# Optimization experiments

Hardware: AMD Instinct MI355X
Metric: run time of the kernel (lower is better)

Reference implementation:

```python
import jax, jax.numpy as jnp
import numpy as np

H = 200  # LSTM hidden size
DT = 48  # tactile dim
DA = 6   # action dim


def setup_inputs() -> dict:
    key = jax.random.key(0)
    ks = jax.random.split(key, 16)
    T, B = 20, 32768
    s = 0.05
    inp = {
        "tactiles": jax.random.normal(ks[0], (T, B, DT), jnp.float32),
        "actions": jax.random.normal(ks[1], (T, B, DA), jnp.float32),
        # lstm1: input 48 -> hidden 200 (PyTorch gate order i,f,g,o)
        "Wih1": jax.random.normal(ks[2], (4 * H, DT), jnp.float32) * s,
        "Whh1": jax.random.normal(ks[3], (4 * H, H), jnp.float32) * s,
        "bih1": jax.random.normal(ks[4], (4 * H,), jnp.float32) * s,
        "bhh1": jax.random.normal(ks[5], (4 * H,), jnp.float32) * s,
        # lstm2: input 248 -> hidden 200
        "Wih2": jax.random.normal(ks[6], (4 * H, H + DT), jnp.float32) * s,
        "Whh2": jax.random.normal(ks[7], (4 * H, H), jnp.float32) * s,
        "bih2": jax.random.normal(ks[8], (4 * H,), jnp.float32) * s,
        "bhh2": jax.random.normal(ks[9], (4 * H,), jnp.float32) * s,
        # fc1: 248 -> 200, fc2: 200 -> 48
        "W1": jax.random.normal(ks[10], (H, H + DT), jnp.float32) * s,
        "b1": jax.random.normal(ks[11], (H,), jnp.float32) * s,
        "W2": jax.random.normal(ks[12], (DT, H), jnp.float32) * s,
        "b2": jax.random.normal(ks[13], (DT,), jnp.float32) * s,
        "context_frames": 10,
    }
    return inp


def _lstm_cell(x, h, c, Wih, Whh, b):
    z = x @ Wih.T + h @ Whh.T + b
    i, f, g, o = jnp.split(z, 4, axis=-1)
    c = jax.nn.sigmoid(f) * c + jax.nn.sigmoid(i) * jnp.tanh(g)
    h = jax.nn.sigmoid(o) * jnp.tanh(c)
    return h, c


def reference(tactiles, actions, Wih1, Whh1, bih1, bhh1, Wih2, Whh2, bih2, bhh2, W1, b1, W2, b2, context_frames):
    T, B, _ = tactiles.shape
    cf = int(context_frames)
    state = actions[0]  # [B, DA]
    bb1 = bih1 + bhh1
    bb2 = bih2 + bhh2

    def tiled(a):
        return jnp.concatenate([a, state, a, state, a, state, a, state], axis=-1)

    def body(carry, inp, prev_tact):
        h1, c1, h2, c2, _ = carry
        act = inp[1] if prev_tact is None else inp
        x1 = inp[0] if prev_tact is None else prev_tact
        h1, c1 = _lstm_cell(x1, h1, c1, Wih1, Whh1, bb1)
        x2 = jnp.concatenate([h1, tiled(act)], axis=-1)  # [B, 248]
        h2, c2 = _lstm_cell(x2, h2, c2, Wih2, Whh2, bb2)
        lp = jnp.concatenate([h2, x1], axis=-1)  # [B, 248]
        out3 = jnp.tanh(lp @ W1.T + b1)
        out4 = jnp.tanh(out3 @ W2.T + b2)
        return (h1, c1, h2, c2, out4)

    def ctx_step(carry, inp):
        return body(carry, inp, None), None

    def pred_step(carry, act):
        new = body(carry, act, carry[4])
        return new, new[4]

    z = jnp.zeros((B, H), tactiles.dtype)
    carry0 = (z, z, z, z, jnp.zeros((B, DT), tactiles.dtype))
    # context phase: indices 0..cf-1 feed ground-truth tactile
    carry, _ = jax.lax.scan(ctx_step, carry0, (tactiles[:cf], actions[1:cf + 1]))
    last_output = carry[4]
    # prediction phase: indices cf..T-2 feed previous prediction
    carry, preds = jax.lax.scan(pred_step, carry, actions[cf + 1:T])
    return jnp.concatenate([last_output[None], preds], axis=0)  # [T-cf, B, 48]
```

## Files before the change

kernel.cpp:

```cpp
#include <hip/hip_runtime.h>


typedef short bf16x8 __attribute__((ext_vector_type(8)));
typedef float f32x16 __attribute__((ext_vector_type(16)));

#define NFRAG    1398
#define FRAG_B2  448
#define FRAG_BF1 1260
#define FRAG_BF2 1372

__device__ __forceinline__ unsigned short f2bf(float f) {
  unsigned int x = __float_as_uint(f);
  x += 0x7fffu + ((x >> 16) & 1u);
  return (unsigned short)(x >> 16);
}
__device__ __forceinline__ float sigf(float x) {
  return __builtin_amdgcn_rcpf(1.f + __expf(-x));
}
__device__ __forceinline__ float tanh_f(float x) {
  float e = __expf(2.f * fabsf(x));
  float t = 1.f - 2.f * __builtin_amdgcn_rcpf(e + 1.f);
  return copysignf(t, x);
}

__device__ __forceinline__ const bf16x8* uni_frag(
    const unsigned short* __restrict__ ws, int frag) {
  const int f = __builtin_amdgcn_readfirstlane(frag);
  return (const bf16x8*)(ws + (size_t)f * 512);
}

__global__ void actp_prep(
    const float* __restrict__ Wih1, const float* __restrict__ Whh1,
    const float* __restrict__ bih1, const float* __restrict__ bhh1,
    const float* __restrict__ Wih2, const float* __restrict__ Whh2,
    const float* __restrict__ bih2, const float* __restrict__ bhh2,
    const float* __restrict__ W1,   const float* __restrict__ W2,
    unsigned short* __restrict__ ws)
{
  const int bid = blockIdx.x, l = threadIdx.x;
  if (bid >= NFRAG) {
    const int idx = (bid - NFRAG) * 64 + l;
    float* bb = (float*)(ws + (size_t)NFRAG * 512);
    if (idx < 800)        bb[idx] = bih1[idx] + bhh1[idx];
    else if (idx < 1600)  bb[idx] = bih2[idx - 800] + bhh2[idx - 800];
    return;
  }
  const int ncol = l & 31;
  const int kb   = (l >> 5) * 8;
  float v[8];
  if (bid < FRAG_B2) {
    int t = bid; const int g = t / 112; t -= g * 112;
    const int jt = t / 16, kc = t % 16;
    const int n = jt * 32 + ncol, row = g * 200 + n;
#pragma unroll
    for (int i = 0; i < 8; ++i) {
      const int k = kc * 16 + kb + i; float val = 0.f;
      if (n < 200) {
        if (kc < 3) val = Wih1[row * 48 + k];
        else { const int kk = k - 48; if (kk < 200) val = Whh1[row * 200 + kk]; }
      }
      v[i] = val;
    }
  } else if (bid < FRAG_BF1) {
    int t = bid - FRAG_B2; const int g = t / 203; t -= g * 203;
    const int jt = t / 29, kc = t % 29;
    const int n = jt * 32 + ncol, row = g * 200 + n;
#pragma unroll
    for (int i = 0; i < 8; ++i) {
      const int k = kc * 16 + kb + i; float val = 0.f;
      if (n < 200) {
        if (kc < 13)      { if (k < 200) val = Wih2[row * 248 + k]; }
        else if (kc < 16) { val = Wih2[row * 248 + 200 + (k - 208)]; }
        else { const int kk = k - 256; if (kk < 200) val = Whh2[row * 200 + kk]; }
      }
      v[i] = val;
    }
  } else if (bid < FRAG_BF2) {
    int t = bid - FRAG_BF1; const int jt = t / 16, kc = t % 16;
    const int n = jt * 32 + ncol;
#pragma unroll
    for (int i = 0; i < 8; ++i) {
      const int k = kc * 16 + kb + i; float val = 0.f;
      if (n < 200) {
        if (kc < 13) { if (k < 200) val = W1[n * 248 + k]; }
        else         val = W1[n * 248 + 200 + (k - 208)];
      }
      v[i] = val;
    }
  } else {
    int t = bid - FRAG_BF2; const int jt = t / 13, kc = t % 13;
    const int n = jt * 32 + ncol;
#pragma unroll
    for (int i = 0; i < 8; ++i) {
      const int k = kc * 16 + kb + i; float val = 0.f;
      if (n < 48 && k < 200) val = W2[n * 200 + k];
      v[i] = val;
    }
  }
  bf16x8 o;
#pragma unroll
  for (int i = 0; i < 8; ++i) o[i] = (short)f2bf(v[i]);
  ((bf16x8*)ws)[(size_t)bid * 64 + l] = o;
}

template<int KC, int C1, int C2>
__device__ __forceinline__ f32x16 gemm1g(
    const unsigned short* __restrict__ A1, int S1,
    const unsigned short* __restrict__ A2, int S2,
    const unsigned short* __restrict__ A3, int S3,
    const bf16x8* __restrict__ B, int lane)
{
  const int r32 = lane & 31, ao = (lane >> 5) * 8;
#define APTR(kc) ((kc) < C1 ? (A1 + r32 * S1 + (kc) * 16 + ao) \
               : ((kc) < C2 ? (A2 + r32 * S2 + ((kc) - C1) * 16 + ao) \
                            : (A3 + r32 * S3 + ((kc) - C2) * 16 + ao)))
  f32x16 acc;
#pragma unroll
  for (int r = 0; r < 16; ++r) acc[r] = 0.f;
  bf16x8 a[4];
#pragma unroll
  for (int p = 0; p < 4 && p < KC; ++p) a[p] = *(const bf16x8*)APTR(p);
  bf16x8 b[8];
#pragma unroll
  for (int p = 0; p < 8 && p < KC; ++p) b[p] = B[(size_t)p * 64 + lane];
#pragma unroll
  for (int kc = 0; kc < KC; ++kc) {
    acc = __builtin_amdgcn_mfma_f32_32x32x16_bf16(a[kc & 3], b[kc & 7], acc, 0, 0, 0);
    if (kc + 4 < KC) a[kc & 3] = *(const bf16x8*)APTR(kc + 4);
    if (kc + 8 < KC) b[kc & 7] = B[(size_t)(kc + 8) * 64 + lane];
  }
#undef APTR
  return acc;
}

__global__ __launch_bounds__(512)
__attribute__((amdgpu_waves_per_eu(2)))
void actp_main(
    const float* __restrict__ tact, const float* __restrict__ act,
    const unsigned short* __restrict__ ws,
    const float* __restrict__ b1v, const float* __restrict__ b2v,
    float* __restrict__ out)
{
  __shared__ unsigned short lds[32768];
  unsigned short* const h1bufA = lds;
  unsigned short* const h1bufB = lds + 7424;
  unsigned short* const h2bufA = lds + 14848;
  unsigned short* const h2bufB = lds + 22272;
  unsigned short* const x1b    = lds + 29696;
  unsigned short* const tld    = lds + 31232;

  const int tid = threadIdx.x, lane = tid & 63, wid = tid >> 6;
  const int q = wid;
  const int l31 = lane & 31, kh = lane >> 5;
  const int jc = q * 32 + l31;
  const size_t rowbase = (size_t)blockIdx.x * 32;

  const float* const bb1 = (const float*)(ws + (size_t)NFRAG * 512);
  const float* const bb2 = bb1 + 800;
  const bool vv = jc < 200;

  for (int i = tid; i < 3712; i += 512) {
    ((unsigned int*)h1bufB)[i] = 0u;
    ((unsigned int*)h2bufB)[i] = 0u;
  }

  float c1[16], c2[16], tmp[16];
#pragma unroll
  for (int r = 0; r < 16; ++r) { c1[r] = 0.f; c2[r] = 0.f; }

  for (int s = 0; s < 19; ++s) {
    if (s < 10 && tid < 192) {
      const int row = tid / 6, ch = tid % 6;
      const float* src = tact + ((size_t)s * 32768 + rowbase + row) * 48 + ch * 8;
      float4 v0 = *(const float4*)src;
      float4 v1 = *(const float4*)(src + 4);
      bf16x8 u;
      u[0] = (short)f2bf(v0.x); u[1] = (short)f2bf(v0.y);
      u[2] = (short)f2bf(v0.z); u[3] = (short)f2bf(v0.w);
      u[4] = (short)f2bf(v1.x); u[5] = (short)f2bf(v1.y);
      u[6] = (short)f2bf(v1.z); u[7] = (short)f2bf(v1.w);
      *(bf16x8*)(x1b + row * 48 + ch * 8) = u;
    }
    if (tid < 64) {
      const int row = tid >> 1, hf = tid & 1;
      const float* pa = act + ((size_t)(s + 1) * 32768 + rowbase + row) * 6;
      const float* ps = act + (rowbase + row) * 6;
      float a6[6], s6[6];
#pragma unroll
      for (int j = 0; j < 6; ++j) { a6[j] = pa[j]; s6[j] = ps[j]; }
#pragma unroll
      for (int k = 0; k < 3; ++k) {
        bf16x8 w;
#pragma unroll
        for (int j = 0; j < 8; ++j) {
          const int c = k * 8 + j;
          const int b6 = c / 6, jj = c % 6;
          w[j] = (short)f2bf((b6 & 1) ? s6[jj] : a6[jj]);
        }
        *(bf16x8*)(tld + row * 48 + hf * 24 + k * 8) = w;
      }
    }
    __syncthreads();

    const int P = s & 1;
    unsigned short* const h1n = P ? h1bufB : h1bufA;
    unsigned short* const h1o = P ? h1bufA : h1bufB;
    unsigned short* const h2n = P ? h2bufB : h2bufA;
    unsigned short* const h2o = P ? h2bufA : h2bufB;

    if (q < 7) {
      {
        const float bf = vv ? bb1[200 + jc] : 0.f;
        f32x16 z = gemm1g<16, 3, 16>(x1b, 48, h1o, 232, h1o, 232,
                                     uni_frag(ws, 112 + q * 16), lane);
#pragma unroll
        for (int r = 0; r < 16; ++r) c1[r] *= sigf(z[r] + bf);
      }
      {
        const float bi = vv ? bb1[jc] : 0.f;
        f32x16 z = gemm1g<16, 3, 16>(x1b, 48, h1o, 232, h1o, 232,
                                     uni_frag(ws, q * 16), lane);
#pragma unroll
        for (int r = 0; r < 16; ++r) tmp[r] = sigf(z[r] + bi);
      }
      {
        const float bg = vv ? bb1[400 + jc] : 0.f;
        f32x16 z = gemm1g<16, 3, 16>(x1b, 48, h1o, 232, h1o, 232,
                                     uni_frag(ws, 224 + q * 16), lane);
#pragma unroll
        for (int r = 0; r < 16; ++r) c1[r] += tmp[r] * tanh_f(z[r] + bg);
      }
      {
        const float bo = vv ? bb1[600 + jc] : 0.f;
        f32x16 z = gemm1g<16, 3, 16>(x1b, 48, h1o, 232, h1o, 232,
                                     uni_frag(ws, 336 + q * 16), lane);
#pragma unroll
        for (int r = 0; r < 16; ++r) {
          const int row = 4 * kh + 8 * (r >> 2) + (r & 3);
          h1n[row * 232 + jc] = f2bf(sigf(z[r] + bo) * tanh_f(c1[r]));
        }
      }
    }
    __syncthreads();

    if (q < 7) {
      {
        const float bf = vv ? bb2[200 + jc] : 0.f;
        f32x16 z = gemm1g<29, 13, 16>(h1n, 232, tld, 48, h2o, 232,
                                      uni_frag(ws, FRAG_B2 + 203 + q * 29), lane);
#pragma unroll
        for (int r = 0; r < 16; ++r) c2[r] *= sigf(z[r] + bf);
      }
      {
        const float bi = vv ? bb2[jc] : 0.f;
        f32x16 z = gemm1g<29, 13, 16>(h1n, 232, tld, 48, h2o, 232,
                                      uni_frag(ws, FRAG_B2 + q * 29), lane);
#pragma unroll
        for (int r = 0; r < 16; ++r) tmp[r] = sigf(z[r] + bi);
      }
      {
        const float bg = vv ? bb2[400 + jc] : 0.f;
        f32x16 z = gemm1g<29, 13, 16>(h1n, 232, tld, 48, h2o, 232,
                                      uni_frag(ws, FRAG_B2 + 406 + q * 29), lane);
#pragma unroll
        for (int r = 0; r < 16; ++r) c2[r] += tmp[r] * tanh_f(z[r] + bg);
      }
      {
        const float bo = vv ? bb2[600 + jc] : 0.f;
        f32x16 z = gemm1g<29, 13, 16>(h1n, 232, tld, 48, h2o, 232,
                                      uni_frag(ws, FRAG_B2 + 609 + q * 29), lane);
#pragma unroll
        for (int r = 0; r < 16; ++r) {
          const int row = 4 * kh + 8 * (r >> 2) + (r & 3);
          h2n[row * 232 + jc] = f2bf(sigf(z[r] + bo) * tanh_f(c2[r]));
        }
      }
    }
    __syncthreads();

    if (s >= 9) {
      unsigned short* const o3 = h1o;
      if (wid < 7) {
        const float br = vv ? b1v[jc] : 0.f;
        f32x16 a = gemm1g<16, 13, 16>(h2n, 232, x1b, 48, x1b, 48,
                                      uni_frag(ws, FRAG_BF1 + wid * 16), lane);
#pragma unroll
        for (int r = 0; r < 16; ++r) {
          const int row = 4 * kh + 8 * (r >> 2) + (r & 3);
          o3[row * 232 + jc] = f2bf(tanh_f(a[r] + br));
        }
      }
      __syncthreads();
      if (wid < 2) {
        const float br = (jc < 48) ? b2v[jc] : 0.f;
        f32x16 a = gemm1g<13, 13, 13>(o3, 232, o3, 232, o3, 232,
                                      uni_frag(ws, FRAG_BF2 + wid * 13), lane);
        if (jc < 48) {
#pragma unroll
          for (int r = 0; r < 16; ++r) {
            const int row = 4 * kh + 8 * (r >> 2) + (r & 3);
            const float v = tanh_f(a[r] + br);
            out[((size_t)(s - 9) * 32768 + rowbase + row) * 48 + jc] = v;
            x1b[row * 48 + jc] = f2bf(v);
          }
        }
      }
      __syncthreads();
    }
  }
}

extern "C" void kernel_launch(void* const* d_in, const int* in_sizes, int n_in,
                              void* d_out, int out_size, void* d_ws, size_t ws_size,
                              hipStream_t stream) {
  const float* tactp = (const float*)d_in[0];
  const float* actp  = (const float*)d_in[1];
  const float* Wih1  = (const float*)d_in[2];
  const float* Whh1  = (const float*)d_in[3];
  const float* bih1  = (const float*)d_in[4];
  const float* bhh1  = (const float*)d_in[5];
  const float* Wih2  = (const float*)d_in[6];
  const float* Whh2  = (const float*)d_in[7];
  const float* bih2  = (const float*)d_in[8];
  const float* bhh2  = (const float*)d_in[9];
  const float* W1    = (const float*)d_in[10];
  const float* b1    = (const float*)d_in[11];
  const float* W2    = (const float*)d_in[12];
  const float* b2    = (const float*)d_in[13];
  unsigned short* ws = (unsigned short*)d_ws;
  float* outp = (float*)d_out;

  actp_prep<<<NFRAG + 25, 64, 0, stream>>>(Wih1, Whh1, bih1, bhh1,
                                           Wih2, Whh2, bih2, bhh2, W1, W2, ws);
  actp_main<<<1024, 512, 0, stream>>>(tactp, actp, ws, b1, b2, outp);
}
```

Baseline: 1.537 ms.

## Process 64 batch rows per block so each weight fragment feeds two MFMAs

Each block now handles 64 batch rows instead of 32. The GEMM helper computes two 32-row accumulator tiles that share every loaded weight fragment, which halves weight-fragment traffic per row and halves the grid to 512 blocks. LDS use doubles to 128 KB of dynamic shared memory, and register pressure rises because cell states and accumulators are duplicated. The A-operand prefetch depth also drops from 4 to 2 chunks. The risks are lower occupancy, possible spills, and fewer blocks to spread across the CUs.

```diff
diff --git a/kernel.cpp b/kernel.cpp
--- a/kernel.cpp
+++ b/kernel.cpp
@@ -104,33 +104,39 @@
 }
 
 template<int KC, int C1, int C2>
-__device__ __forceinline__ f32x16 gemm1g(
+__device__ __forceinline__ void gemm2m(
     const unsigned short* __restrict__ A1, int S1,
     const unsigned short* __restrict__ A2, int S2,
     const unsigned short* __restrict__ A3, int S3,
-    const bf16x8* __restrict__ B, int lane)
+    const bf16x8* __restrict__ B, f32x16* acc, int lane)
 {
   const int r32 = lane & 31, ao = (lane >> 5) * 8;
-#define APTR(kc) ((kc) < C1 ? (A1 + r32 * S1 + (kc) * 16 + ao) \
-               : ((kc) < C2 ? (A2 + r32 * S2 + ((kc) - C1) * 16 + ao) \
-                            : (A3 + r32 * S3 + ((kc) - C2) * 16 + ao)))
-  f32x16 acc;
-#pragma unroll
-  for (int r = 0; r < 16; ++r) acc[r] = 0.f;
-  bf16x8 a[4];
-#pragma unroll
-  for (int p = 0; p < 4 && p < KC; ++p) a[p] = *(const bf16x8*)APTR(p);
+#define APTR(kc, t) ((kc) < C1 ? (A1 + ((t) * 32 + r32) * S1 + (kc) * 16 + ao) \
+               : ((kc) < C2 ? (A2 + ((t) * 32 + r32) * S2 + ((kc) - C1) * 16 + ao) \
+                            : (A3 + ((t) * 32 + r32) * S3 + ((kc) - C2) * 16 + ao)))
+#pragma unroll
+  for (int r = 0; r < 16; ++r) { acc[0][r] = 0.f; acc[1][r] = 0.f; }
+  bf16x8 a0[2], a1[2];
+  a0[0] = *(const bf16x8*)APTR(0, 0);
+  a1[0] = *(const bf16x8*)APTR(0, 1);
+  if (KC > 1) {
+    a0[1] = *(const bf16x8*)APTR(1, 0);
+    a1[1] = *(const bf16x8*)APTR(1, 1);
+  }
   bf16x8 b[8];
 #pragma unroll
   for (int p = 0; p < 8 && p < KC; ++p) b[p] = B[(size_t)p * 64 + lane];
 #pragma unroll
   for (int kc = 0; kc < KC; ++kc) {
-    acc = __builtin_amdgcn_mfma_f32_32x32x16_bf16(a[kc & 3], b[kc & 7], acc, 0, 0, 0);
-    if (kc + 4 < KC) a[kc & 3] = *(const bf16x8*)APTR(kc + 4);
+    acc[0] = __builtin_amdgcn_mfma_f32_32x32x16_bf16(a0[kc & 1], b[kc & 7], acc[0], 0, 0, 0);
+    acc[1] = __builtin_amdgcn_mfma_f32_32x32x16_bf16(a1[kc & 1], b[kc & 7], acc[1], 0, 0, 0);
+    if (kc + 2 < KC) {
+      a0[kc & 1] = *(const bf16x8*)APTR(kc + 2, 0);
+      a1[kc & 1] = *(const bf16x8*)APTR(kc + 2, 1);
+    }
     if (kc + 8 < KC) b[kc & 7] = B[(size_t)(kc + 8) * 64 + lane];
   }
 #undef APTR
-  return acc;
 }
 
 __global__ __launch_bounds__(512)
@@ -141,35 +147,37 @@
     const float* __restrict__ b1v, const float* __restrict__ b2v,
     float* __restrict__ out)
 {
-  __shared__ unsigned short lds[32768];
+  extern __shared__ unsigned short lds[];
   unsigned short* const h1bufA = lds;
-  unsigned short* const h1bufB = lds + 7424;
-  unsigned short* const h2bufA = lds + 14848;
-  unsigned short* const h2bufB = lds + 22272;
-  unsigned short* const x1b    = lds + 29696;
-  unsigned short* const tld    = lds + 31232;
+  unsigned short* const h1bufB = lds + 14848;
+  unsigned short* const h2bufA = lds + 29696;
+  unsigned short* const h2bufB = lds + 44544;
+  unsigned short* const x1b    = lds + 59392;
+  unsigned short* const tld    = lds + 62464;
 
   const int tid = threadIdx.x, lane = tid & 63, wid = tid >> 6;
   const int q = wid;
   const int l31 = lane & 31, kh = lane >> 5;
   const int jc = q * 32 + l31;
-  const size_t rowbase = (size_t)blockIdx.x * 32;
+  const size_t rowbase = (size_t)blockIdx.x * 64;
 
   const float* const bb1 = (const float*)(ws + (size_t)NFRAG * 512);
   const float* const bb2 = bb1 + 800;
   const bool vv = jc < 200;
 
-  for (int i = tid; i < 3712; i += 512) {
+  for (int i = tid; i < 7424; i += 512) {
     ((unsigned int*)h1bufB)[i] = 0u;
     ((unsigned int*)h2bufB)[i] = 0u;
   }
 
-  float c1[16], c2[16], tmp[16];
-#pragma unroll
-  for (int r = 0; r < 16; ++r) { c1[r] = 0.f; c2[r] = 0.f; }
+  float c1[2][16], c2[2][16], tmp[2][16];
+#pragma unroll
+  for (int t = 0; t < 2; ++t)
+#pragma unroll
+    for (int r = 0; r < 16; ++r) { c1[t][r] = 0.f; c2[t][r] = 0.f; }
 
   for (int s = 0; s < 19; ++s) {
-    if (s < 10 && tid < 192) {
+    if (s < 10 && tid < 384) {
       const int row = tid / 6, ch = tid % 6;
       const float* src = tact + ((size_t)s * 32768 + rowbase + row) * 48 + ch * 8;
       float4 v0 = *(const float4*)src;
@@ -181,7 +189,7 @@
       u[6] = (short)f2bf(v1.z); u[7] = (short)f2bf(v1.w);
       *(bf16x8*)(x1b + row * 48 + ch * 8) = u;
     }
-    if (tid < 64) {
+    if (tid < 128) {
       const int row = tid >> 1, hf = tid & 1;
       const float* pa = act + ((size_t)(s + 1) * 32768 + rowbase + row) * 6;
       const float* ps = act + (rowbase + row) * 6;
@@ -209,71 +217,89 @@
     unsigned short* const h2o = P ? h2bufA : h2bufB;
 
     if (q < 7) {
+      f32x16 z[2];
       {
         const float bf = vv ? bb1[200 + jc] : 0.f;
-        f32x16 z = gemm1g<16, 3, 16>(x1b, 48, h1o, 232, h1o, 232,
-                                     uni_frag(ws, 112 + q * 16), lane);
-#pragma unroll
-        for (int r = 0; r < 16; ++r) c1[r] *= sigf(z[r] + bf);
+        gemm2m<16, 3, 16>(x1b, 48, h1o, 232, h1o, 232,
+                          uni_frag(ws, 112 + q * 16), z, lane);
+#pragma unroll
+        for (int t = 0; t < 2; ++t)
+#pragma unroll
+          for (int r = 0; r < 16; ++r) c1[t][r] *= sigf(z[t][r] + bf);
       }
       {
         const float bi = vv ? bb1[jc] : 0.f;
-        f32x16 z = gemm1g<16, 3, 16>(x1b, 48, h1o, 232, h1o, 232,
-                                     uni_frag(ws, q * 16), lane);
-#pragma unroll
-        for (int r = 0; r < 16; ++r) tmp[r] = sigf(z[r] + bi);
+        gemm2m<16, 3, 16>(x1b, 48, h1o, 232, h1o, 232,
+                          uni_frag(ws, q * 16), z, lane);
+#pragma unroll
+        for (int t = 0; t < 2; ++t)
+#pragma unroll
+          for (int r = 0; r < 16; ++r) tmp[t][r] = sigf(z[t][r] + bi);
       }
       {
         const float bg = vv ? bb1[400 + jc] : 0.f;
-        f32x16 z = gemm1g<16, 3, 16>(x1b, 48, h1o, 232, h1o, 232,
-                                     uni_frag(ws, 224 + q * 16), lane);
-#pragma unroll
-        for (int r = 0; r < 16; ++r) c1[r] += tmp[r] * tanh_f(z[r] + bg);
+        gemm2m<16, 3, 16>(x1b, 48, h1o, 232, h1o, 232,
+                          uni_frag(ws, 224 + q * 16), z, lane);
+#pragma unroll
+        for (int t = 0; t < 2; ++t)
+#pragma unroll
+          for (int r = 0; r < 16; ++r) c1[t][r] += tmp[t][r] * tanh_f(z[t][r] + bg);
       }
       {
         const float bo = vv ? bb1[600 + jc] : 0.f;
-        f32x16 z = gemm1g<16, 3, 16>(x1b, 48, h1o, 232, h1o, 232,
-                                     uni_frag(ws, 336 + q * 16), lane);
-#pragma unroll
-        for (int r = 0; r < 16; ++r) {
-          const int row = 4 * kh + 8 * (r >> 2) + (r & 3);
-          h1n[row * 232 + jc] = f2bf(sigf(z[r] + bo) * tanh_f(c1[r]));
-        }
+        gemm2m<16, 3, 16>(x1b, 48, h1o, 232, h1o, 232,
+                          uni_frag(ws, 336 + q * 16), z, lane);
+#pragma unroll
+        for (int t = 0; t < 2; ++t)
+#pragma unroll
+          for (int r = 0; r < 16; ++r) {
+            const int row = t * 32 + 4 * kh + 8 * (r >> 2) + (r & 3);
+            h1n[row * 232 + jc] = f2bf(sigf(z[t][r] + bo) * tanh_f(c1[t][r]));
+          }
       }
     }
     __syncthreads();
 
     if (q < 7) {
+      f32x16 z[2];
       {
         const float bf = vv ? bb2[200 + jc] : 0.f;
-        f32x16 z = gemm1g<29, 13, 16>(h1n, 232, tld, 48, h2o, 232,
-                                      uni_frag(ws, FRAG_B2 + 203 + q * 29), lane);
-#pragma unroll
-        for (int r = 0; r < 16; ++r) c2[r] *= sigf(z[r] + bf);
+        gemm2m<29, 13, 16>(h1n, 232, tld, 48, h2o, 232,
+                           uni_frag(ws, FRAG_B2 + 203 + q * 29), z, lane);
+#pragma unroll
+        for (int t = 0; t < 2; ++t)
+#pragma unroll
+          for (int r = 0; r < 16; ++r) c2[t][r] *= sigf(z[t][r] + bf);
       }
       {
         const float bi = vv ? bb2[jc] : 0.f;
-        f32x16 z = gemm1g<29, 13, 16>(h1n, 232, tld, 48, h2o, 232,
-                                      uni_frag(ws, FRAG_B2 + q * 29), lane);
-#pragma unroll
-        for (int r = 0; r < 16; ++r) tmp[r] = sigf(z[r] + bi);
+        gemm2m<29, 13, 16>(h1n, 232, tld, 48, h2o, 232,
+                           uni_frag(ws, FRAG_B2 + q * 29), z, lane);
+#pragma unroll
+        for (int t = 0; t < 2; ++t)
+#pragma unroll
+          for (int r = 0; r < 16; ++r) tmp[t][r] = sigf(z[t][r] + bi);
       }
       {
         const float bg = vv ? bb2[400 + jc] : 0.f;
-        f32x16 z = gemm1g<29, 13, 16>(h1n, 232, tld, 48, h2o, 232,
-                                      uni_frag(ws, FRAG_B2 + 406 + q * 29), lane);
-#pragma unroll
-        for (int r = 0; r < 16; ++r) c2[r] += tmp[r] * tanh_f(z[r] + bg);
+        gemm2m<29, 13, 16>(h1n, 232, tld, 48, h2o, 232,
+                           uni_frag(ws, FRAG_B2 + 406 + q * 29), z, lane);
+#pragma unroll
+        for (int t = 0; t < 2; ++t)
+#pragma unroll
+          for (int r = 0; r < 16; ++r) c2[t][r] += tmp[t][r] * tanh_f(z[t][r] + bg);
       }
       {
         const float bo = vv ? bb2[600 + jc] : 0.f;
-        f32x16 z = gemm1g<29, 13, 16>(h1n, 232, tld, 48, h2o, 232,
-                                      uni_frag(ws, FRAG_B2 + 609 + q * 29), lane);
-#pragma unroll
-        for (int r = 0; r < 16; ++r) {
-          const int row = 4 * kh + 8 * (r >> 2) + (r & 3);
-          h2n[row * 232 + jc] = f2bf(sigf(z[r] + bo) * tanh_f(c2[r]));
-        }
+        gemm2m<29, 13, 16>(h1n, 232, tld, 48, h2o, 232,
+                           uni_frag(ws, FRAG_B2 + 609 + q * 29), z, lane);
+#pragma unroll
+        for (int t = 0; t < 2; ++t)
+#pragma unroll
+          for (int r = 0; r < 16; ++r) {
+            const int row = t * 32 + 4 * kh + 8 * (r >> 2) + (r & 3);
+            h2n[row * 232 + jc] = f2bf(sigf(z[t][r] + bo) * tanh_f(c2[t][r]));
+          }
       }
     }
     __syncthreads();
@@ -281,28 +307,34 @@
     if (s >= 9) {
       unsigned short* const o3 = h1o;
       if (wid < 7) {
+        f32x16 a[2];
         const float br = vv ? b1v[jc] : 0.f;
-        f32x16 a = gemm1g<16, 13, 16>(h2n, 232, x1b, 48, x1b, 48,
-                                      uni_frag(ws, FRAG_BF1 + wid * 16), lane);
-#pragma unroll
-        for (int r = 0; r < 16; ++r) {
-          const int row = 4 * kh + 8 * (r >> 2) + (r & 3);
-          o3[row * 232 + jc] = f2bf(tanh_f(a[r] + br));
-        }
+        gemm2m<16, 13, 16>(h2n, 232, x1b, 48, x1b, 48,
+                           uni_frag(ws, FRAG_BF1 + wid * 16), a, lane);
+#pragma unroll
+        for (int t = 0; t < 2; ++t)
+#pragma unroll
+          for (int r = 0; r < 16; ++r) {
+            const int row = t * 32 + 4 * kh + 8 * (r >> 2) + (r & 3);
+            o3[row * 232 + jc] = f2bf(tanh_f(a[t][r] + br));
+          }
       }
       __syncthreads();
       if (wid < 2) {
+        f32x16 a[2];
         const float br = (jc < 48) ? b2v[jc] : 0.f;
-        f32x16 a = gemm1g<13, 13, 13>(o3, 232, o3, 232, o3, 232,
-                                      uni_frag(ws, FRAG_BF2 + wid * 13), lane);
+        gemm2m<13, 13, 13>(o3, 232, o3, 232, o3, 232,
+                           uni_frag(ws, FRAG_BF2 + wid * 13), a, lane);
         if (jc < 48) {
 #pragma unroll
-          for (int r = 0; r < 16; ++r) {
-            const int row = 4 * kh + 8 * (r >> 2) + (r & 3);
-            const float v = tanh_f(a[r] + br);
-            out[((size_t)(s - 9) * 32768 + rowbase + row) * 48 + jc] = v;
-            x1b[row * 48 + jc] = f2bf(v);
-          }
+          for (int t = 0; t < 2; ++t)
+#pragma unroll
+            for (int r = 0; r < 16; ++r) {
+              const int row = t * 32 + 4 * kh + 8 * (r >> 2) + (r & 3);
+              const float v = tanh_f(a[t][r] + br);
+              out[((size_t)(s - 9) * 32768 + rowbase + row) * 48 + jc] = v;
+              x1b[row * 48 + jc] = f2bf(v);
+            }
         }
       }
       __syncthreads();
@@ -330,7 +362,10 @@
   unsigned short* ws = (unsigned short*)d_ws;
   float* outp = (float*)d_out;
 
+  hipFuncSetAttribute((const void*)actp_main,
+                      hipFuncAttributeMaxDynamicSharedMemorySize, 131072);
+
   actp_prep<<<NFRAG + 25, 64, 0, stream>>>(Wih1, Whh1, bih1, bhh1,
                                            Wih2, Whh2, bih2, bhh2, W1, W2, ws);
-  actp_main<<<1024, 512, 0, stream>>>(tactp, actp, ws, b1, b2, outp);
-}
+  actp_main<<<512, 512, 131072, stream>>>(tactp, actp, ws, b1, b2, outp);
+}
```

New measurement: 3.057 ms. +98.8%, slower.
